# Performance work log

Hardware: AMD Instinct MI355X
Metric: run time of the kernel (lower is better)

Reference implementation:

```python
import jax, jax.numpy as jnp
import numpy as np
from jax import lax

BETA = 0.3

def setup_inputs() -> dict:
    key = jax.random.key(0)
    ks = jax.random.split(key, 5)
    B, C, H, W = 1, 64, 96, 96
    x = jax.random.normal(ks[0], (B, C, H, W), dtype=jnp.float32)
    # d_conv: Conv2d(C, C, k=3, stride=1, padding=2, dilation=2)
    dW = jax.random.normal(ks[1], (C, C, 3, 3), dtype=jnp.float32) * 0.05
    db = jax.random.normal(ks[2], (C,), dtype=jnp.float32) * 0.05
    # conv: Conv2d(C, C, k=1)
    cW = jax.random.normal(ks[3], (C, C, 1, 1), dtype=jnp.float32) * 0.1
    cb = jax.random.normal(ks[4], (C,), dtype=jnp.float32) * 0.05
    return {"x": x, "dW": dW, "db": db, "cW": cW, "cb": cb}

def _conv(x, w, b, padding, dilation):
    y = lax.conv_general_dilated(
        x, w, window_strides=(1, 1),
        padding=[(padding, padding), (padding, padding)],
        rhs_dilation=(dilation, dilation),
        dimension_numbers=("NCHW", "OIHW", "NCHW"))
    return y + b[None, :, None, None]

def reference(x, dW, db, cW, cb):
    B, C, H, W = x.shape
    HW = H * W
    y = _conv(x, dW, db, padding=2, dilation=2)   # (B,C,H,W), same d_conv used for q and k
    v = _conv(x, cW, cb, padding=0, dilation=1).reshape(B, HW, C)
    # NOTE: torch uses raw .reshape (not transpose) for q — faithful here.
    q = y.reshape(B, HW, C)
    k = y.reshape(B, C, HW)
    qk = jnp.einsum("bnc,bcm->bnm", q, k)         # (B,HW,HW)
    qk = jnp.where(jnp.abs(qk) > BETA, qk, 0.0)   # threshold mask (qk*mask)
    att = jax.nn.softmax(qk, axis=-1)
    att = jnp.einsum("bnm,bmc->bnc", att, v)      # (B,HW,C)
    att = att.swapaxes(1, 2).reshape(B, C, H, W)
    return x + att
```

## Files before the change

kernel.cpp:

```cpp
#include <hip/hip_runtime.h>
#include <hip/hip_bf16.h>

#define CC 64
#define HW 9216
#define IMG 96
#define SPLITS 16
#define SPLEN 576
#define ITERS 9
#define LOG2E 1.44269504f

typedef _Float16 f16;
typedef __attribute__((ext_vector_type(8))) _Float16 f16x8;
typedef __attribute__((ext_vector_type(4))) _Float16 f16x4;
typedef __attribute__((ext_vector_type(4))) float f32x4;
typedef __attribute__((ext_vector_type(16))) float f32x16;
typedef __attribute__((ext_vector_type(4))) unsigned int u32x4;

__global__ __launch_bounds__(256) void prepad_kernel(
    const float* __restrict__ x, const float* __restrict__ dW, const float* __restrict__ cW,
    f16* __restrict__ xt, f16* __restrict__ dWt, f16* __restrict__ cWt)
{
    __shared__ float tile[64][65];
    const int t = threadIdx.x;
    if (blockIdx.x >= 157) {
        const int wb = blockIdx.x - 157;
        #pragma unroll
        for (int j = 0; j < 4; ++j) {
            int idx = wb * 1024 + j * 256 + t;
            if (idx < 36864) {
                float val = dW[idx];
                int co = idx / 576;
                int r = idx - co * 576;
                int ci = r / 9, tap = r - ci * 9;
                dWt[tap * 4096 + co * 64 + ci] = (f16)val;
            } else {
                int c = idx - 36864;
                cWt[c] = (f16)cW[c];
            }
        }
        return;
    }
    const int p0 = blockIdx.x * 64;
    const int pl = t & 63;
    const int p = p0 + pl;
    int r = p / 100, c = p % 100;
    bool interior = (r >= 2) && (r < 98) && (c >= 2) && (c < 98);
    int img = (r - 2) * IMG + (c - 2);
    #pragma unroll
    for (int j = 0; j < 16; ++j) {
        int ci = j * 4 + (t >> 6);
        tile[pl][ci] = interior ? x[ci * HW + img] : 0.f;
    }
    __syncthreads();
    const int row16 = t >> 4, chunk = t & 15;
    #pragma unroll
    for (int j = 0; j < 4; ++j) {
        int row = j * 16 + row16;
        int pr = p0 + row;
        if (pr < 10000) {
            f16x4 hv = {(f16)tile[row][chunk * 4 + 0], (f16)tile[row][chunk * 4 + 1],
                        (f16)tile[row][chunk * 4 + 2], (f16)tile[row][chunk * 4 + 3]};
            *(f16x4*)&xt[pr * 64 + chunk * 4] = hv;
        }
    }
}

__global__ __launch_bounds__(256) void conv_mfma_kernel(
    const f16* __restrict__ xt, const f16* __restrict__ dWt, const float* __restrict__ db,
    const f16* __restrict__ cWt, const float* __restrict__ cb,
    f16* __restrict__ yq, f16* __restrict__ kt, f16* __restrict__ vt)
{
    const int b = blockIdx.x;
    const int mblk = b >> 2, cog = b & 3;
    const int co0 = cog * 16;
    const int t = threadIdx.x;
    const int w = t >> 6, L = t & 63, g = L >> 4, c16 = L & 15;

    f16x8 Bf[9][2], Bv[2];
    #pragma unroll
    for (int tap = 0; tap < 9; ++tap)
        #pragma unroll
        for (int kc = 0; kc < 2; ++kc)
            Bf[tap][kc] = *(const f16x8*)&dWt[(tap * 64 + co0 + c16) * 64 + g * 8 + kc * 32];
    #pragma unroll
    for (int kc = 0; kc < 2; ++kc)
        Bv[kc] = *(const f16x8*)&cWt[(co0 + c16) * 64 + g * 8 + kc * 32];

    const int ms = mblk * 64 + w * 16;
    const int h = ms / IMG, wc = ms % IMG;
    const int pb = (h + 2) * 100 + (wc + 2) + c16;

    f32x4 accY = (f32x4){0.f, 0.f, 0.f, 0.f};
    f32x4 accV = (f32x4){0.f, 0.f, 0.f, 0.f};

    #pragma unroll
    for (int tap = 0; tap < 9; ++tap) {
        int kh = tap / 3, kw = tap % 3;
        int toff = (2 * kh - 2) * 100 + (2 * kw - 2);
        const f16* ap = xt + (pb + toff) * 64;
        f16x8 A0 = *(const f16x8*)(ap + g * 8);
        f16x8 A1 = *(const f16x8*)(ap + g * 8 + 32);
        accY = __builtin_amdgcn_mfma_f32_16x16x32_f16(A0, Bf[tap][0], accY, 0, 0, 0);
        accY = __builtin_amdgcn_mfma_f32_16x16x32_f16(A1, Bf[tap][1], accY, 0, 0, 0);
        if (tap == 4) {
            accV = __builtin_amdgcn_mfma_f32_16x16x32_f16(A0, Bv[0], accV, 0, 0, 0);
            accV = __builtin_amdgcn_mfma_f32_16x16x32_f16(A1, Bv[1], accV, 0, 0, 0);
        }
    }

    const float dbv = db[co0 + c16], cbv = cb[co0 + c16];
    f16 hy[4];
    #pragma unroll
    for (int j = 0; j < 4; ++j) hy[j] = (f16)(accY[j] + dbv);
    *(f16x4*)&yq[(co0 + c16) * HW + ms + 4 * g] = (f16x4){hy[0], hy[1], hy[2], hy[3]};
    #pragma unroll
    for (int j = 0; j < 4; ++j)
        kt[(ms + 4 * g + j) * 64 + co0 + c16] = hy[j];
    #pragma unroll
    for (int j = 0; j < 4; ++j) {
        int m = ms + 4 * g + j;
        vt[(m & 63) * HW + (co0 + c16) * 144 + (m >> 6)] = (f16)(accV[j] + cbv);
    }
}

__global__ __launch_bounds__(256, 4) void attn_kernel(
    const f16* __restrict__ kt, const f16* __restrict__ vt, const f16* __restrict__ yq,
    f16* __restrict__ acc_ws, float* __restrict__ m_ws, float* __restrict__ l_ws)
{
    __shared__ f16 sKT[64 * 64];
    __shared__ f16 sVT[64 * 64];
    __shared__ float sAL[4 * 32];

    const int t = threadIdx.x;
    const int L = t & 63, w = t >> 6;
    const int l5 = L >> 5, l31 = L & 31;
    const int x7 = l31 & 7;
    const int qb = blockIdx.x >> 4, sp = blockIdx.x & (SPLITS - 1);
    const int n0 = qb * 128;
    const int mbase = sp * SPLEN;
    float* alw = (float*)sAL + w * 32;

    f16x8 qf[4];
    #pragma unroll
    for (int kc = 0; kc < 4; ++kc)
        qf[kc] = *(const f16x8*)(yq + (n0 + w * 32 + l31) * 64 + kc * 16 + l5 * 8);

    float mi = -1e30f, li = 0.f;
    f32x16 acc[2];
    #pragma unroll
    for (int ct = 0; ct < 2; ++ct)
        #pragma unroll
        for (int r = 0; r < 16; ++r) acc[ct][r] = 0.f;

    for (int it = 0; it < ITERS; ++it) {
        const int m0 = mbase + it * 64;
        __syncthreads();
        #pragma unroll
        for (int rep = 0; rep < 2; ++rep) {
            int idx = t + rep * 256;
            int row = idx >> 3, ch = idx & 7;
            int dst = row * 64 + ((ch ^ (row & 7)) << 3);
            *(uint4*)&sKT[dst] = *(const uint4*)&kt[(m0 + row) * 64 + ch * 8];
            *(uint4*)&sVT[dst] = *(const uint4*)&vt[row * HW + m0 + ch * 8];
        }
        __syncthreads();

        f32x16 st[2];
        #pragma unroll
        for (int kt2 = 0; kt2 < 2; ++kt2) {
            f32x16 d;
            #pragma unroll
            for (int r = 0; r < 16; ++r) d[r] = 0.f;
            #pragma unroll
            for (int kc = 0; kc < 4; ++kc) {
                f16x8 af = *(const f16x8*)&sKT[(kt2 * 32 + l31) * 64 + ((((kc << 1) | l5) ^ x7) << 3)];
                d = __builtin_amdgcn_mfma_f32_32x32x16_f16(af, qf[kc], d, 0, 0, 0);
            }
            st[kt2] = d;
        }
        #pragma unroll
        for (int kt2 = 0; kt2 < 2; ++kt2)
            #pragma unroll
            for (int r = 0; r < 16; ++r)
                st[kt2][r] = (fabsf(st[kt2][r]) > 0.3f) ? st[kt2][r] : 0.f;

        float q8[8];
        #pragma unroll
        for (int kt2 = 0; kt2 < 2; ++kt2)
            #pragma unroll
            for (int rq = 0; rq < 4; ++rq)
                q8[kt2 * 4 + rq] = fmaxf(fmaxf(st[kt2][rq * 4 + 0], st[kt2][rq * 4 + 1]),
                                         fmaxf(st[kt2][rq * 4 + 2], st[kt2][rq * 4 + 3]));
        float mx = fmaxf(fmaxf(fmaxf(q8[0], q8[1]), fmaxf(q8[2], q8[3])),
                         fmaxf(fmaxf(q8[4], q8[5]), fmaxf(q8[6], q8[7])));
        mx = fmaxf(mx, __shfl_xor(mx, 32, 64));
        float mnew = fmaxf(mi, mx);
        unsigned long long inc = __ballot(mnew > mi);
        float nL = mnew * LOG2E;

        float ls = 0.f;
        unsigned int u[2][4][2];
        #pragma unroll
        for (int kt2 = 0; kt2 < 2; ++kt2)
            #pragma unroll
            for (int rq = 0; rq < 4; ++rq) {
                float p0 = __builtin_amdgcn_exp2f(fmaf(st[kt2][rq * 4 + 0], LOG2E, -nL));
                float p1 = __builtin_amdgcn_exp2f(fmaf(st[kt2][rq * 4 + 1], LOG2E, -nL));
                float p2 = __builtin_amdgcn_exp2f(fmaf(st[kt2][rq * 4 + 2], LOG2E, -nL));
                float p3 = __builtin_amdgcn_exp2f(fmaf(st[kt2][rq * 4 + 3], LOG2E, -nL));
                ls += (p0 + p1) + (p2 + p3);
                u[kt2][rq][0] = __builtin_bit_cast(unsigned int, __builtin_amdgcn_cvt_pkrtz(p0, p1));
                u[kt2][rq][1] = __builtin_bit_cast(unsigned int, __builtin_amdgcn_cvt_pkrtz(p2, p3));
            }

        if (inc) {
            float alpha = __builtin_amdgcn_exp2f(mi * LOG2E - nL);
            li = li * alpha + ls;
            if (l5 == 0) alw[l31] = alpha;
            f32x4 aj[4];
            #pragma unroll
            for (int rq = 0; rq < 4; ++rq)
                aj[rq] = *(const f32x4*)&alw[rq * 8 + l5 * 4];
            #pragma unroll
            for (int ct = 0; ct < 2; ++ct)
                #pragma unroll
                for (int r = 0; r < 16; ++r)
                    acc[ct][r] *= aj[r >> 2][r & 3];
        } else {
            li += ls;
        }
        mi = mnew;

        #pragma unroll
        for (int kc = 0; kc < 4; ++kc) {
            const int kt2 = kc >> 1;
            const int rq0 = (kc & 1) * 2, rq1 = rq0 + 1;
            auto rA = __builtin_amdgcn_permlane32_swap(
                (int)u[kt2][rq0][0], (int)u[kt2][rq1][0], false, false);
            auto rB = __builtin_amdgcn_permlane32_swap(
                (int)u[kt2][rq0][1], (int)u[kt2][rq1][1], false, false);
            u32x4 pw = {(unsigned int)rA[0], (unsigned int)rB[0],
                        (unsigned int)rA[1], (unsigned int)rB[1]};
            f16x8 pa = __builtin_bit_cast(f16x8, pw);
            #pragma unroll
            for (int ct = 0; ct < 2; ++ct) {
                int vrow = ct * 32 + l31;
                f16x8 vb = *(const f16x8*)&sVT[vrow * 64 + ((((kc << 1) | l5) ^ x7) << 3)];
                acc[ct] = __builtin_amdgcn_mfma_f32_32x32x16_f16(pa, vb, acc[ct], 0, 0, 0);
            }
        }
    }

    float li_tot = li + __shfl_xor(li, 32, 64);

    const int base = blockIdx.x;
    #pragma unroll
    for (int ct = 0; ct < 2; ++ct)
        #pragma unroll
        for (int r = 0; r < 16; ++r) {
            int ql = w * 32 + (r & 3) + 8 * (r >> 2) + 4 * l5;
            int c  = ct * 32 + l31;
            acc_ws[base * 8192 + ql * 64 + c] = (f16)acc[ct][r];
        }
    if (l5 == 0) {
        m_ws[base * 128 + w * 32 + l31] = mi;
        l_ws[base * 128 + w * 32 + l31] = li_tot;
    }
}

__global__ __launch_bounds__(256) void merge_kernel(
    const f16* __restrict__ acc_ws, const float* __restrict__ m_ws, const float* __restrict__ l_ws,
    const float* __restrict__ x, float* __restrict__ out)
{
    __shared__ float wsh[SPLITS * 16];
    __shared__ float att[64 * 17];
    const int b = blockIdx.x;
    const int row0 = b * 16;
    const int qb = row0 >> 7;
    const int ql0 = row0 & 127;
    const int t = threadIdx.x;
    if (t < 16) {
        int ql = ql0 + t;
        float ms = -1e30f;
        float mv[SPLITS];
        #pragma unroll
        for (int sp = 0; sp < SPLITS; ++sp) {
            mv[sp] = m_ws[(qb * SPLITS + sp) * 128 + ql];
            ms = fmaxf(ms, mv[sp]);
        }
        float Lsum = 0.f, ev[SPLITS];
        #pragma unroll
        for (int sp = 0; sp < SPLITS; ++sp) {
            ev[sp] = __builtin_amdgcn_exp2f((mv[sp] - ms) * LOG2E);
            Lsum += l_ws[(qb * SPLITS + sp) * 128 + ql] * ev[sp];
        }
        float inv = 1.f / Lsum;
        #pragma unroll
        for (int sp = 0; sp < SPLITS; ++sp)
            wsh[sp * 16 + t] = ev[sp] * inv;
    }
    __syncthreads();
    for (int i = t; i < 1024; i += 256) {
        int rr = i >> 6, c = i & 63;
        float v = 0.f;
        #pragma unroll
        for (int sp = 0; sp < SPLITS; ++sp)
            v += (float)acc_ws[(qb * SPLITS + sp) * 8192 + (ql0 + rr) * 64 + c] * wsh[sp * 16 + rr];
        att[c * 17 + rr] = v;
    }
    __syncthreads();
    for (int i = t; i < 1024; i += 256) {
        int c = i >> 4, r = i & 15;
        int idx = c * HW + row0 + r;
        out[idx] = x[idx] + att[c * 17 + r];
    }
}

extern "C" void kernel_launch(void* const* d_in, const int* in_sizes, int n_in,
                              void* d_out, int out_size, void* d_ws, size_t ws_size,
                              hipStream_t stream)
{
    const float* x  = (const float*)d_in[0];
    const float* dW = (const float*)d_in[1];
    const float* db = (const float*)d_in[2];
    const float* cW = (const float*)d_in[3];
    const float* cb = (const float*)d_in[4];
    float* out = (float*)d_out;

    char* ws = (char*)d_ws;
    f16* kt     = (f16*)(ws);
    f16* yq     = (f16*)(ws + 1179648);
    f16* vt     = (f16*)(ws + 2359296);
    f16* xt     = (f16*)(ws + 3538944);
    f16* dWt    = (f16*)(ws + 4818944);
    f16* cWt    = (f16*)(ws + 4892672);
    f16* acc_ws = (f16*)(ws + 4900864);
    float* m_ws = (float*)(ws + 23775232);
    float* l_ws = (float*)(ws + 24365056);

    prepad_kernel<<<dim3(197), dim3(256), 0, stream>>>(x, dW, cW, xt, dWt, cWt);
    conv_mfma_kernel<<<dim3(576), dim3(256), 0, stream>>>(xt, dWt, db, cWt, cb, yq, kt, vt);
    attn_kernel<<<dim3(72 * SPLITS), dim3(256), 0, stream>>>(kt, vt, yq, acc_ws, m_ws, l_ws);
    merge_kernel<<<dim3(576), dim3(256), 0, stream>>>(acc_ws, m_ws, l_ws, x, out);
}
```

Before: 136.3 us.

## Prefetch K/V tiles into registers, lazy softmax rescale, smaller conv/prepad blocks

The attention kernel now loads the next K/V tile into registers while computing the current one, so global latency overlaps with MFMA work. The online softmax only rescales the accumulator when the row max grows by more than a fixed threshold (lazy rescaling), then does one final correction against the true max. The prepad and conv kernels switch to smaller blocks and more of them (32 positions per prepad block, 64-thread conv blocks) to raise parallelism. The risks are extra register pressure in attention and the possibility of f16 overflow in the unnormalized accumulator, which the threshold is meant to bound.

Result: slower. 146.4 us (+7.4%).

```diff
diff --git a/kernel.cpp b/kernel.cpp
--- a/kernel.cpp
+++ b/kernel.cpp
@@ -8,6 +8,7 @@
 #define SPLEN 576
 #define ITERS 9
 #define LOG2E 1.44269504f
+#define RESC 5.545f
 
 typedef _Float16 f16;
 typedef __attribute__((ext_vector_type(8))) _Float16 f16x8;
@@ -20,10 +21,10 @@
     const float* __restrict__ x, const float* __restrict__ dW, const float* __restrict__ cW,
     f16* __restrict__ xt, f16* __restrict__ dWt, f16* __restrict__ cWt)
 {
-    __shared__ float tile[64][65];
+    __shared__ float tile[32][65];
     const int t = threadIdx.x;
-    if (blockIdx.x >= 157) {
-        const int wb = blockIdx.x - 157;
+    if (blockIdx.x >= 313) {
+        const int wb = blockIdx.x - 313;
         #pragma unroll
         for (int j = 0; j < 4; ++j) {
             int idx = wb * 1024 + j * 256 + t;
@@ -40,21 +41,21 @@
         }
         return;
     }
-    const int p0 = blockIdx.x * 64;
-    const int pl = t & 63;
+    const int p0 = blockIdx.x * 32;
+    const int pl = t & 31;
     const int p = p0 + pl;
     int r = p / 100, c = p % 100;
     bool interior = (r >= 2) && (r < 98) && (c >= 2) && (c < 98);
     int img = (r - 2) * IMG + (c - 2);
     #pragma unroll
-    for (int j = 0; j < 16; ++j) {
-        int ci = j * 4 + (t >> 6);
+    for (int j = 0; j < 8; ++j) {
+        int ci = j * 8 + (t >> 5);
         tile[pl][ci] = interior ? x[ci * HW + img] : 0.f;
     }
     __syncthreads();
     const int row16 = t >> 4, chunk = t & 15;
     #pragma unroll
-    for (int j = 0; j < 4; ++j) {
+    for (int j = 0; j < 2; ++j) {
         int row = j * 16 + row16;
         int pr = p0 + row;
         if (pr < 10000) {
@@ -65,16 +66,16 @@
     }
 }
 
-__global__ __launch_bounds__(256) void conv_mfma_kernel(
+__global__ __launch_bounds__(64) void conv_mfma_kernel(
     const f16* __restrict__ xt, const f16* __restrict__ dWt, const float* __restrict__ db,
     const f16* __restrict__ cWt, const float* __restrict__ cb,
     f16* __restrict__ yq, f16* __restrict__ kt, f16* __restrict__ vt)
 {
     const int b = blockIdx.x;
-    const int mblk = b >> 2, cog = b & 3;
+    const int tile = b >> 2, cog = b & 3;
     const int co0 = cog * 16;
-    const int t = threadIdx.x;
-    const int w = t >> 6, L = t & 63, g = L >> 4, c16 = L & 15;
+    const int L = threadIdx.x;
+    const int g = L >> 4, c16 = L & 15;
 
     f16x8 Bf[9][2], Bv[2];
     #pragma unroll
@@ -86,7 +87,7 @@
     for (int kc = 0; kc < 2; ++kc)
         Bv[kc] = *(const f16x8*)&cWt[(co0 + c16) * 64 + g * 8 + kc * 32];
 
-    const int ms = mblk * 64 + w * 16;
+    const int ms = tile * 16;
     const int h = ms / IMG, wc = ms % IMG;
     const int pb = (h + 2) * 100 + (wc + 2) + c16;
 
@@ -140,30 +141,42 @@
     const int mbase = sp * SPLEN;
     float* alw = (float*)sAL + w * 32;
 
+    const int srow0 = t >> 3, sch = t & 7;
+    const int srow1 = srow0 + 32;
+    const int dst0 = srow0 * 64 + ((sch ^ (srow0 & 7)) << 3);
+    const int dst1 = srow1 * 64 + ((sch ^ (srow1 & 7)) << 3);
+
     f16x8 qf[4];
     #pragma unroll
     for (int kc = 0; kc < 4; ++kc)
         qf[kc] = *(const f16x8*)(yq + (n0 + w * 32 + l31) * 64 + kc * 16 + l5 * 8);
 
-    float mi = -1e30f, li = 0.f;
+    float mi = -1e30f, mtrue = -1e30f, li = 0.f;
     f32x16 acc[2];
     #pragma unroll
     for (int ct = 0; ct < 2; ++ct)
         #pragma unroll
         for (int r = 0; r < 16; ++r) acc[ct][r] = 0.f;
 
+    uint4 rK0 = *(const uint4*)&kt[(mbase + srow0) * 64 + sch * 8];
+    uint4 rK1 = *(const uint4*)&kt[(mbase + srow1) * 64 + sch * 8];
+    uint4 rV0 = *(const uint4*)&vt[srow0 * HW + mbase + sch * 8];
+    uint4 rV1 = *(const uint4*)&vt[srow1 * HW + mbase + sch * 8];
+
     for (int it = 0; it < ITERS; ++it) {
-        const int m0 = mbase + it * 64;
+        const int m0n = mbase + (it + 1) * 64;
         __syncthreads();
-        #pragma unroll
-        for (int rep = 0; rep < 2; ++rep) {
-            int idx = t + rep * 256;
-            int row = idx >> 3, ch = idx & 7;
-            int dst = row * 64 + ((ch ^ (row & 7)) << 3);
-            *(uint4*)&sKT[dst] = *(const uint4*)&kt[(m0 + row) * 64 + ch * 8];
-            *(uint4*)&sVT[dst] = *(const uint4*)&vt[row * HW + m0 + ch * 8];
-        }
+        *(uint4*)&sKT[dst0] = rK0;
+        *(uint4*)&sKT[dst1] = rK1;
+        *(uint4*)&sVT[dst0] = rV0;
+        *(uint4*)&sVT[dst1] = rV1;
         __syncthreads();
+        if (it + 1 < ITERS) {
+            rK0 = *(const uint4*)&kt[(m0n + srow0) * 64 + sch * 8];
+            rK1 = *(const uint4*)&kt[(m0n + srow1) * 64 + sch * 8];
+            rV0 = *(const uint4*)&vt[srow0 * HW + m0n + sch * 8];
+            rV1 = *(const uint4*)&vt[srow1 * HW + m0n + sch * 8];
+        }
 
         f32x16 st[2];
         #pragma unroll
@@ -194,9 +207,26 @@
         float mx = fmaxf(fmaxf(fmaxf(q8[0], q8[1]), fmaxf(q8[2], q8[3])),
                          fmaxf(fmaxf(q8[4], q8[5]), fmaxf(q8[6], q8[7])));
         mx = fmaxf(mx, __shfl_xor(mx, 32, 64));
-        float mnew = fmaxf(mi, mx);
-        unsigned long long inc = __ballot(mnew > mi);
-        float nL = mnew * LOG2E;
+        mtrue = fmaxf(mtrue, mx);
+
+        unsigned long long need = __ballot(mx > mi + RESC);
+        if (need) {
+            float mnew = fmaxf(mi, mx);
+            float alpha = __builtin_amdgcn_exp2f((mi - mnew) * LOG2E);
+            li *= alpha;
+            if (l5 == 0) alw[l31] = alpha;
+            f32x4 aj[4];
+            #pragma unroll
+            for (int rq = 0; rq < 4; ++rq)
+                aj[rq] = *(const f32x4*)&alw[rq * 8 + l5 * 4];
+            #pragma unroll
+            for (int ct = 0; ct < 2; ++ct)
+                #pragma unroll
+                for (int r = 0; r < 16; ++r)
+                    acc[ct][r] *= aj[r >> 2][r & 3];
+            mi = mnew;
+        }
+        const float nL = mi * LOG2E;
 
         float ls = 0.f;
         unsigned int u[2][4][2];
@@ -212,24 +242,7 @@
                 u[kt2][rq][0] = __builtin_bit_cast(unsigned int, __builtin_amdgcn_cvt_pkrtz(p0, p1));
                 u[kt2][rq][1] = __builtin_bit_cast(unsigned int, __builtin_amdgcn_cvt_pkrtz(p2, p3));
             }
-
-        if (inc) {
-            float alpha = __builtin_amdgcn_exp2f(mi * LOG2E - nL);
-            li = li * alpha + ls;
-            if (l5 == 0) alw[l31] = alpha;
-            f32x4 aj[4];
-            #pragma unroll
-            for (int rq = 0; rq < 4; ++rq)
-                aj[rq] = *(const f32x4*)&alw[rq * 8 + l5 * 4];
-            #pragma unroll
-            for (int ct = 0; ct < 2; ++ct)
-                #pragma unroll
-                for (int r = 0; r < 16; ++r)
-                    acc[ct][r] *= aj[r >> 2][r & 3];
-        } else {
-            li += ls;
-        }
-        mi = mnew;
+        li += ls;
 
         #pragma unroll
         for (int kc = 0; kc < 4; ++kc) {
@@ -251,7 +264,19 @@
         }
     }
 
+    float fsc = __builtin_amdgcn_exp2f((mi - mtrue) * LOG2E);
+    li *= fsc;
     float li_tot = li + __shfl_xor(li, 32, 64);
+    if (l5 == 0) alw[l31] = fsc;
+    f32x4 fj[4];
+    #pragma unroll
+    for (int rq = 0; rq < 4; ++rq)
+        fj[rq] = *(const f32x4*)&alw[rq * 8 + l5 * 4];
+    #pragma unroll
+    for (int ct = 0; ct < 2; ++ct)
+        #pragma unroll
+        for (int r = 0; r < 16; ++r)
+            acc[ct][r] *= fj[r >> 2][r & 3];
 
     const int base = blockIdx.x;
     #pragma unroll
@@ -263,7 +288,7 @@
             acc_ws[base * 8192 + ql * 64 + c] = (f16)acc[ct][r];
         }
     if (l5 == 0) {
-        m_ws[base * 128 + w * 32 + l31] = mi;
+        m_ws[base * 128 + w * 32 + l31] = mtrue;
         l_ws[base * 128 + w * 32 + l31] = li_tot;
     }
 }
@@ -338,8 +363,8 @@
     float* m_ws = (float*)(ws + 23775232);
     float* l_ws = (float*)(ws + 24365056);
 
-    prepad_kernel<<<dim3(197), dim3(256), 0, stream>>>(x, dW, cW, xt, dWt, cWt);
-    conv_mfma_kernel<<<dim3(576), dim3(256), 0, stream>>>(xt, dWt, db, cWt, cb, yq, kt, vt);
+    prepad_kernel<<<dim3(353), dim3(256), 0, stream>>>(x, dW, cW, xt, dWt, cWt);
+    conv_mfma_kernel<<<dim3(2304), dim3(64), 0, stream>>>(xt, dWt, db, cWt, cb, yq, kt, vt);
     attn_kernel<<<dim3(72 * SPLITS), dim3(256), 0, stream>>>(kt, vt, yq, acc_ws, m_ws, l_ws);
     merge_kernel<<<dim3(576), dim3(256), 0, stream>>>(acc_ws, m_ws, l_ws, x, out);
 }
```
